# Kernel tuning notes

Measured on AMD Instinct MI355X. Metric: run time of the kernel, lower is better.

Reference implementation:

```python
import jax, jax.numpy as jnp
import numpy as np

NHID, NHEAD, HEAD_DIM, U = 512, 16, 64, 3  # U = unfold_size (hardcoded 3 in original)
B, L = 8, 2048
D = NHEAD * HEAD_DIM  # 1024


def setup_inputs() -> dict:
    key = jax.random.key(0)
    ks = jax.random.split(key, 9)
    s = 0.02
    return {
        "x": jax.random.normal(ks[0], (B, NHID, L, 1), jnp.float32),
        "wq": jax.random.normal(ks[1], (NHID, D), jnp.float32) * s,
        "bq": jnp.zeros((D,), jnp.float32),
        "wk": jax.random.normal(ks[2], (NHID, D), jnp.float32) * s,
        "bk": jnp.zeros((D,), jnp.float32),
        "wv": jax.random.normal(ks[3], (NHID, D), jnp.float32) * s,
        "bv": jnp.zeros((D,), jnp.float32),
        "wo": jax.random.normal(ks[4], (D, NHID), jnp.float32) * s,
        "bo": jnp.zeros((NHID,), jnp.float32),
    }


def _unfold(t):
    # t: (B, D, L). Replicates tf.image.extract_patches (ksize 3, SAME, zero pad)
    # followed by the original's reshape (B,L,1,D,3) -- which reinterprets the
    # window-major flat layout (w*D + c) as (c', w') -- then transpose to
    # (B, D, 3, L) and reshape to (B, nhead, head_dim, 3, L).
    b, d, l = t.shape
    tt = jnp.transpose(t, (0, 2, 1))                  # (B, L, D)
    tp = jnp.pad(tt, ((0, 0), (1, 1), (0, 0)))        # SAME zero padding along L
    p = jnp.stack([tp[:, w:w + l, :] for w in range(U)], axis=2)  # (B, L, 3, D), flat idx = w*D + c
    p = p.reshape(b, l, d, U)                         # faithful reinterpreting reshape
    p = jnp.transpose(p, (0, 2, 3, 1))                # (B, D, 3, L)
    return p.reshape(b, NHEAD, HEAD_DIM, U, l)


def reference(x, wq, bq, wk, bk, wv, bv, wo, bo):
    b, c, l, _ = x.shape
    xs = x[..., 0]                                    # (B, C, L)
    # 1x1 convs (channels_first) == channel matmuls
    q = jnp.einsum('bcl,cd->bdl', xs, wq) + bq[None, :, None]
    k = jnp.einsum('bcl,cd->bdl', xs, wk) + bk[None, :, None]
    v = jnp.einsum('bcl,cd->bdl', xs, wv) + bv[None, :, None]
    q = q.reshape(b, NHEAD, HEAD_DIM, 1, l)           # (B, nh, hd, 1, L)
    k = _unfold(k)                                    # (B, nh, hd, 3, L)
    v = _unfold(v)
    scale = jnp.sqrt(jnp.asarray(HEAD_DIM, x.dtype))
    alphas = jnp.sum(q * k, axis=2, keepdims=True) / scale  # (B, nh, 1, 3, L)
    alphas = jax.nn.softmax(alphas, axis=3)
    att = jnp.sum(alphas * v, axis=3)                 # (B, nh, hd, L)
    # faithful to original: transpose then reinterpreting reshape to (B, D, L)
    att = jnp.transpose(att, (0, 1, 3, 2)).reshape(b, D, l)
    ret = jnp.einsum('bdl,dc->bcl', att, wo) + bo[None, :, None]
    return ret[..., None]                             # (B, nhid, L, 1)
```

## Files before the change

kernel.cpp:

```cpp
#include <hip/hip_runtime.h>

typedef _Float16 f16_t;
typedef _Float16 f16x2 __attribute__((ext_vector_type(2)));
typedef _Float16 f16x8 __attribute__((ext_vector_type(8)));
typedef float floatx4 __attribute__((ext_vector_type(4)));
typedef unsigned int u32;
typedef const __attribute__((address_space(1))) unsigned int* gptr_as1;
typedef __attribute__((address_space(3))) unsigned int* lptr_as3;

#define B_ 8
#define C_ 512
#define L_ 2048
#define D_ 1024
#define H_ 16

static __device__ __forceinline__ f16x2 bc2(u32 v) { return __builtin_bit_cast(f16x2, v); }
static __device__ __forceinline__ u32 cb2(f16x2 v) { return __builtin_bit_cast(u32, v); }

#define SCHEDB() __builtin_amdgcn_sched_barrier(0)

__global__ __launch_bounds__(256) void _MSA1_ktransf2h(const float* __restrict__ in,
                                                       f16_t* __restrict__ out,
                                                       int R, int C) {
  size_t zoff = (size_t)blockIdx.z * R * C;
  in += zoff; out += zoff;
  __shared__ f16_t tile[64][65];
  int r0 = blockIdx.y * 64, c0 = blockIdx.x * 64;
  int t = threadIdx.x;
  #pragma unroll
  for (int i = 0; i < 16; ++i) {
    int idx = t + i * 256;
    int r = idx >> 6, c = idx & 63;
    tile[c][r] = (f16_t)in[(size_t)(r0 + r) * C + (c0 + c)];
  }
  __syncthreads();
  #pragma unroll
  for (int i = 0; i < 16; ++i) {
    int idx = t + i * 256;
    int r = idx >> 6, c = idx & 63;
    out[(size_t)(c0 + r) * R + (r0 + c)] = tile[r][c];
  }
}

__global__ __launch_bounds__(256) void _MSA1_kprep(
    const float* __restrict__ wq, const float* __restrict__ wk,
    const float* __restrict__ wv, const float* __restrict__ wo,
    const float* __restrict__ bq, const float* __restrict__ bk,
    const float* __restrict__ bv,
    f16_t* __restrict__ wT3, f16_t* __restrict__ woT, float* __restrict__ bias3) {
  const int x = blockIdx.x, y = blockIdx.y;
  const int t = threadIdx.x;
  if (x == 128) {
    if (y == 0) {
      for (int i = t; i < 1024; i += 256) {
        bias3[i] = bq[i];
        bias3[1024 + i] = bk[i];
        bias3[2048 + i] = bv[i];
      }
    }
    return;
  }
  __shared__ f16_t tile[64][65];
  const float* in; f16_t* out; int R, C, r0, c0;
  if (y < 3) {
    R = 512; C = 1024;
    in = (y == 0) ? wq : (y == 1) ? wk : wv;
    out = wT3 + (size_t)y * 524288;
    r0 = (x >> 4) * 64; c0 = (x & 15) * 64;
  } else {
    R = 1024; C = 512;
    in = wo; out = woT;
    r0 = (x >> 3) * 64; c0 = (x & 7) * 64;
  }
  #pragma unroll
  for (int i = 0; i < 16; ++i) {
    int idx = t + i * 256;
    int r = idx >> 6, c = idx & 63;
    tile[c][r] = (f16_t)in[(size_t)(r0 + r) * C + (c0 + c)];
  }
  __syncthreads();
  #pragma unroll
  for (int i = 0; i < 16; ++i) {
    int idx = t + i * 256;
    int r = idx >> 6, c = idx & 63;
    out[(size_t)(c0 + r) * R + (r0 + c)] = tile[r][c];
  }
}

template <int K>
__global__ __launch_bounds__(512, 2) void _MSA1_kgemm8(
    const f16_t* __restrict__ A, const f16_t* __restrict__ Bt,
    const float* __restrict__ bias, f16_t* __restrict__ Cd0,
    int M, int N, long sB, long sC) {
  constexpr int KT = K / 64;
  const f16_t* Bz = Bt + (size_t)blockIdx.z * sB;
  const int m0 = blockIdx.y * 256, n0 = blockIdx.x * 256;

  union __align__(16) ShU {
    f16_t AB[8][8192];
    f16_t Ep[64][264];
  };
  __shared__ ShU sh;

  const int t = threadIdx.x;
  const int lane = t & 63;
  const int wid = t >> 6;
  const int wm = wid & 1, wn = wid >> 1;
  const int mh = wm * 128, nh = wn * 64;
  const int fm = lane & 15, fq = lane >> 4;
  const int srcswz = ((t & 3) ^ ((t >> 2) & 3) ^ ((t >> 4) & 3)) * 8;
  const int colf = ((fq ^ (fm & 3) ^ ((fm >> 2) & 3)) * 8);

  floatx4 acc[8][4];
  #pragma unroll
  for (int i = 0; i < 8; ++i)
    #pragma unroll
    for (int j = 0; j < 4; ++j) {
      floatx4 z4 = {0.f, 0.f, 0.f, 0.f};
      acc[i][j] = z4;
    }

  auto SG = [&](int T, int ab, int kk) {
    const int d = T & 1;
    const f16_t* src = ab ? Bz : A;
    const int base0 = ab ? n0 : m0;
    char* ldsb = (char*)&sh.AB[(d * 2 + ab) * 2 + kk][0];
    #pragma unroll
    for (int j = 0; j < 2; ++j) {
      int idx = j * 512 + t;
      int r = idx >> 2;
      const f16_t* g = src + (size_t)(base0 + r) * K + T * 64 + kk * 32 + srcswz;
      __builtin_amdgcn_global_load_lds((gptr_as1)(const void*)g,
          (lptr_as3)(void*)(ldsb + idx * 16), 16, 0, 0);
    }
  };
  auto LDA4 = [&](f16x8* af, int d, int kk, int mhalf) {
    #pragma unroll
    for (int m2 = 0; m2 < 4; ++m2)
      af[m2] = *(const f16x8*)&sh.AB[(d * 2 + 0) * 2 + kk]
                  [(mh + mhalf * 64 + m2 * 16 + fm) * 32 + colf];
  };
  auto LDB4 = [&](f16x8* bf, int d, int kk) {
    #pragma unroll
    for (int nt = 0; nt < 4; ++nt)
      bf[nt] = *(const f16x8*)&sh.AB[(d * 2 + 1) * 2 + kk]
                  [(nh + nt * 16 + fm) * 32 + colf];
  };
  auto MM = [&](const f16x8* af, const f16x8* bf, int mhalf) {
    __builtin_amdgcn_s_setprio(1);
    #pragma unroll
    for (int m2 = 0; m2 < 4; ++m2)
      #pragma unroll
      for (int nt = 0; nt < 4; ++nt)
        acc[mhalf * 4 + m2][nt] = __builtin_amdgcn_mfma_f32_16x16x32_f16(
            af[m2], bf[nt], acc[mhalf * 4 + m2][nt], 0, 0, 0);
    __builtin_amdgcn_s_setprio(0);
  };

  SG(0, 1, 0); SG(0, 0, 0); SG(0, 1, 1); SG(0, 0, 1);
  SG(1, 1, 0); SG(1, 0, 0); SG(1, 1, 1);
  SCHEDB();
  asm volatile("s_waitcnt vmcnt(10)" ::: "memory");
  __builtin_amdgcn_s_barrier();
  SCHEDB();

  f16x8 af[4], bfr[4];
  #pragma unroll
  for (int i = 0; i < KT; ++i) {
    const int d = i & 1;
    LDB4(bfr, d, 0);
    LDA4(af, d, 0, 0);
    SCHEDB();
    __builtin_amdgcn_s_barrier();
    asm volatile("s_waitcnt lgkmcnt(0)" ::: "memory");
    SCHEDB();
    if (i + 1 < KT) SG(i + 1, 0, 1);
    MM(af, bfr, 0);
    LDA4(af, d, 0, 1);
    SCHEDB();
    if (i == KT - 1) {
      asm volatile("s_waitcnt vmcnt(0)" ::: "memory");
    } else {
      asm volatile("s_waitcnt vmcnt(8)" ::: "memory");
    }
    __builtin_amdgcn_s_barrier();
    asm volatile("s_waitcnt lgkmcnt(0)" ::: "memory");
    SCHEDB();
    if (i + 2 < KT) SG(i + 2, 1, 0);
    MM(af, bfr, 1);
    LDB4(bfr, d, 1);
    LDA4(af, d, 1, 0);
    SCHEDB();
    __builtin_amdgcn_s_barrier();
    asm volatile("s_waitcnt lgkmcnt(0)" ::: "memory");
    SCHEDB();
    if (i + 2 < KT) SG(i + 2, 0, 0);
    MM(af, bfr, 0);
    LDA4(af, d, 1, 1);
    SCHEDB();
    if (i + 1 < KT) {
      asm volatile("s_waitcnt vmcnt(8)" ::: "memory");
    }
    __builtin_amdgcn_s_barrier();
    asm volatile("s_waitcnt lgkmcnt(0)" ::: "memory");
    SCHEDB();
    if (i + 2 < KT) SG(i + 2, 1, 1);
    MM(af, bfr, 1);
  }
  __syncthreads();

  f16_t* Cd = Cd0 + (size_t)blockIdx.z * sC;
  #pragma unroll
  for (int p = 0; p < 4; ++p) {
    if (p) __syncthreads();
    if (wm == (p >> 1)) {
      #pragma unroll
      for (int m2 = 0; m2 < 4; ++m2) {
        int mt = (p & 1) * 4 + m2;
        float bv4[4];
        #pragma unroll
        for (int r = 0; r < 4; ++r)
          bv4[r] = bias[m0 + p * 64 + m2 * 16 + fq * 4 + r];
        #pragma unroll
        for (int nt = 0; nt < 4; ++nt) {
          int col = nh + nt * 16 + fm;
          #pragma unroll
          for (int r = 0; r < 4; ++r) {
            int row = m2 * 16 + fq * 4 + r;
            sh.Ep[row][col] = (f16_t)(acc[mt][nt][r] + bv4[r]);
          }
        }
      }
    }
    __syncthreads();
    #pragma unroll
    for (int ii = 0; ii < 8; ++ii) {
      int chunk = ii * 512 + t;
      int row = chunk >> 6, c8 = chunk & 63;
      uint2 val = *(const uint2*)&sh.Ep[row][c8 * 4];
      *(uint2*)&Cd[(size_t)(m0 + p * 64 + row) * N + n0 + c8 * 4] = val;
    }
  }
}

template <bool F32OUT, int K>
__global__ __launch_bounds__(256, 2) void _MSA1_kgemm(
    const f16_t* __restrict__ A, const f16_t* __restrict__ Bt,
    const float* __restrict__ bias, void* __restrict__ Cdv,
    int M, int N, long sA, long sB, long sC) {
  A  += (size_t)blockIdx.z * sA;
  Bt += (size_t)blockIdx.z * sB;
  const int m0 = blockIdx.y * 256, n0 = blockIdx.x * 128;

  union __align__(16) ShU {
    struct { f16_t As[3][256][32]; f16_t Bs[3][128][32]; } ab;
    f16_t Ep[F32OUT ? 1 : 64][132];
  };
  __shared__ ShU sh;

  const int t = threadIdx.x;
  const int lane = t & 63, w = t >> 6;
  const int mh = (w & 1) * 128, nh = (w >> 1) * 64;
  const int fm = lane & 15, fq = lane >> 4;
  const int srcswz = ((t & 3) ^ ((t >> 2) & 3) ^ ((t >> 4) & 3)) * 8;
  const int colf = ((fq ^ (fm & 3) ^ ((fm >> 2) & 3)) * 8);

  floatx4 acc[8][4];
  #pragma unroll
  for (int i = 0; i < 8; ++i)
    #pragma unroll
    for (int j = 0; j < 4; ++j) {
      floatx4 z4 = {0.f, 0.f, 0.f, 0.f};
      acc[i][j] = z4;
    }

  auto STAGE = [&](int kt, int bi) {
    #pragma unroll
    for (int j = 0; j < 4; ++j) {
      int r = (j * 256 + t) >> 2;
      const f16_t* ga = A + (size_t)(m0 + r) * K + kt + srcswz;
      __builtin_amdgcn_global_load_lds((gptr_as1)(const void*)ga,
          (lptr_as3)(void*)((char*)&sh.ab.As[bi][0][0] + j * 4096 + w * 1024), 16, 0, 0);
    }
    #pragma unroll
    for (int j = 0; j < 2; ++j) {
      int r = (j * 256 + t) >> 2;
      const f16_t* gb = Bt + (size_t)(n0 + r) * K + kt + srcswz;
      __builtin_amdgcn_global_load_lds((gptr_as1)(const void*)gb,
          (lptr_as3)(void*)((char*)&sh.ab.Bs[bi][0][0] + j * 4096 + w * 1024), 16, 0, 0);
    }
  };

  STAGE(0, 0);
  STAGE(32, 1);
  SCHEDB();
  asm volatile("s_waitcnt vmcnt(6)" ::: "memory");
  __builtin_amdgcn_s_barrier();
  SCHEDB();

  int bcur = 0;
  for (int kt = 0; kt < K; kt += 32) {
    if (kt + 64 < K) {
      int bi = bcur + 2; if (bi >= 3) bi -= 3;
      STAGE(kt + 64, bi);
    }
    f16x8 af[8], bfr[4];
    #pragma unroll
    for (int mt = 0; mt < 8; ++mt)
      af[mt] = *(const f16x8*)&sh.ab.As[bcur][mh + mt * 16 + fm][colf];
    #pragma unroll
    for (int nt = 0; nt < 4; ++nt)
      bfr[nt] = *(const f16x8*)&sh.ab.Bs[bcur][nh + nt * 16 + fm][colf];
    __builtin_amdgcn_s_setprio(1);
    #pragma unroll
    for (int mt = 0; mt < 8; ++mt)
      #pragma unroll
      for (int nt = 0; nt < 4; ++nt)
        acc[mt][nt] = __builtin_amdgcn_mfma_f32_16x16x32_f16(
            af[mt], bfr[nt], acc[mt][nt], 0, 0, 0);
    __builtin_amdgcn_s_setprio(0);
    if (kt + 32 < K) {
      SCHEDB();
      if (kt + 64 < K)
        asm volatile("s_waitcnt vmcnt(6) lgkmcnt(0)" ::: "memory");
      else
        asm volatile("s_waitcnt vmcnt(0) lgkmcnt(0)" ::: "memory");
      __builtin_amdgcn_s_barrier();
      SCHEDB();
    }
    bcur = (bcur == 2) ? 0 : bcur + 1;
  }
  __syncthreads();

  if (F32OUT) {
    float* Cd = (float*)Cdv + (size_t)blockIdx.z * sC;
    #pragma unroll
    for (int mt = 0; mt < 8; ++mt) {
      float bv4[4];
      #pragma unroll
      for (int r = 0; r < 4; ++r)
        bv4[r] = bias[m0 + mh + mt * 16 + fq * 4 + r];
      #pragma unroll
      for (int nt = 0; nt < 4; ++nt) {
        int col = n0 + nh + nt * 16 + fm;
        #pragma unroll
        for (int r = 0; r < 4; ++r) {
          int row = m0 + mh + mt * 16 + fq * 4 + r;
          Cd[(size_t)row * N + col] = acc[mt][nt][r] + bv4[r];
        }
      }
    }
  } else {
    f16_t* Cd = (f16_t*)Cdv + (size_t)blockIdx.z * sC;
    #pragma unroll
    for (int p = 0; p < 4; ++p) {
      if (p) __syncthreads();
      if ((w & 1) == (p >> 1)) {
        #pragma unroll
        for (int mt2 = 0; mt2 < 4; ++mt2) {
          int mt = (p & 1) * 4 + mt2;
          float bv4[4];
          #pragma unroll
          for (int r = 0; r < 4; ++r)
            bv4[r] = bias[m0 + p * 64 + mt2 * 16 + fq * 4 + r];
          #pragma unroll
          for (int nt = 0; nt < 4; ++nt) {
            int col = nh + nt * 16 + fm;
            #pragma unroll
            for (int r = 0; r < 4; ++r) {
              int row = mt2 * 16 + fq * 4 + r;
              sh.Ep[row][col] = (f16_t)(acc[mt][nt][r] + bv4[r]);
            }
          }
        }
      }
      __syncthreads();
      #pragma unroll
      for (int i = 0; i < 8; ++i) {
        int chunk = i * 256 + t;
        int row = chunk >> 5, c8 = chunk & 31;
        uint2 val = *(const uint2*)&sh.Ep[row][c8 * 4];
        *(uint2*)&Cd[(size_t)(m0 + p * 64 + row) * N + n0 + c8 * 4] = val;
      }
    }
  }
}

__global__ __launch_bounds__(256) void _MSA1_kattn6(const f16_t* __restrict__ qkv,
                                                    f16_t* __restrict__ attT) {
  const int t = threadIdx.x;
  const int lane = t & 63;
  const int wid = __builtin_amdgcn_readfirstlane(t >> 6);
  const int hb = blockIdx.x;
  const int h = hb & 15, b = hb >> 4;
  const int chi = blockIdx.y;
  const int lbase = chi * 256;
  const int l0 = lbase + lane * 4;
  const size_t plane = (size_t)D_ * L_;
  const f16_t* base = qkv + (size_t)b * 3 * plane;

  __shared__ uint2 sred[4][3][64];
  __shared__ __align__(16) f16_t tile2[2048][8];

  const f16_t* qp = base + (size_t)(h * 64 + wid * 16) * L_ + l0;
  const f16_t* kpl = base + plane;
  const f16_t* vpl = base + 2 * plane;
  const int g0 = h * 192 + wid * 48;

  f16x2 sLo[3], sHi[3];
  #pragma unroll
  for (int w = 0; w < 3; ++w) { f16x2 z = {(f16_t)0, (f16_t)0}; sLo[w] = z; sHi[w] = z; }

  #pragma unroll
  for (int dd = 0; dd < 16; ++dd) {
    uint2 qw = *(const uint2*)(qp + (size_t)dd * L_);
    f16x2 qlo = bc2(qw.x), qhi = bc2(qw.y);
    #pragma unroll
    for (int w = 0; w < 3; ++w) {
      int g = g0 + 3 * dd + w;
      int c = g & 1023;
      int o = (g >> 10) - 1;
      uint2 kw = *(const uint2*)(kpl + (size_t)c * L_ + (l0 + o));
      if (o < 0 && l0 == 0) kw.x &= 0xFFFF0000u;
      if (o > 0 && l0 == 2044) kw.y &= 0x0000FFFFu;
      sLo[w] = bc2(kw.x) * qlo + sLo[w];
      sHi[w] = bc2(kw.y) * qhi + sHi[w];
    }
  }
  #pragma unroll
  for (int w = 0; w < 3; ++w) {
    uint2 v; v.x = cb2(sLo[w]); v.y = cb2(sHi[w]);
    sred[wid][w][lane] = v;
  }
  __syncthreads();

  float sc[4][3];
  #pragma unroll
  for (int j = 0; j < 3; ++j) {
    uint2 r0 = sred[0][j][lane], r1 = sred[1][j][lane];
    uint2 r2 = sred[2][j][lane], r3 = sred[3][j][lane];
    f16x2 lo = (bc2(r0.x) + bc2(r1.x)) + (bc2(r2.x) + bc2(r3.x));
    f16x2 hi = (bc2(r0.y) + bc2(r1.y)) + (bc2(r2.y) + bc2(r3.y));
    sc[0][j] = (float)lo.x * 0.125f;
    sc[1][j] = (float)lo.y * 0.125f;
    sc[2][j] = (float)hi.x * 0.125f;
    sc[3][j] = (float)hi.y * 0.125f;
  }
  f16_t ef[4][3];
  #pragma unroll
  for (int li = 0; li < 4; ++li) {
    float mx = fmaxf(sc[li][0], fmaxf(sc[li][1], sc[li][2]));
    float e0 = __expf(sc[li][0] - mx), e1 = __expf(sc[li][1] - mx), e2 = __expf(sc[li][2] - mx);
    float inv = 1.f / (e0 + e1 + e2);
    ef[li][0] = (f16_t)(e0 * inv); ef[li][1] = (f16_t)(e1 * inv); ef[li][2] = (f16_t)(e2 * inv);
  }
  f16x2 eLo[3], eHi[3];
  #pragma unroll
  for (int w = 0; w < 3; ++w) {
    f16x2 a = {ef[0][w], ef[1][w]}; eLo[w] = a;
    f16x2 b2 = {ef[2][w], ef[3][w]}; eHi[w] = b2;
  }

  const int llb = (lane & 7) * 256 + wid * 16;
  const int jcol = lane >> 3;
  #pragma unroll
  for (int dd = 0; dd < 16; ++dd) {
    f16x2 aLo = {(f16_t)0, (f16_t)0}, aHi = {(f16_t)0, (f16_t)0};
    #pragma unroll
    for (int w = 0; w < 3; ++w) {
      int g = g0 + 3 * dd + w;
      int c = g & 1023;
      int o = (g >> 10) - 1;
      uint2 vw = *(const uint2*)(vpl + (size_t)c * L_ + (l0 + o));
      if (o < 0 && l0 == 0) vw.x &= 0xFFFF0000u;
      if (o > 0 && l0 == 2044) vw.y &= 0x0000FFFFu;
      aLo = bc2(vw.x) * eLo[w] + aLo;
      aHi = bc2(vw.y) * eHi[w] + aHi;
    }
    const int llq = llb + dd;
    tile2[llq +   0][jcol] = aLo.x;
    tile2[llq +  64][jcol] = aLo.y;
    tile2[llq + 128][jcol] = aHi.x;
    tile2[llq + 192][jcol] = aHi.y;
  }
  __syncthreads();

  f16_t* ob = attT + (size_t)b * L_ * D_ + h * 64 + chi * 8;
  #pragma unroll
  for (int i = 0; i < 8; ++i) {
    int ll = i * 256 + t;
    uint4 val = *(const uint4*)&tile2[ll][0];
    *(uint4*)(ob + (size_t)ll * D_) = val;
  }
}

extern "C" void kernel_launch(void* const* d_in, const int* in_sizes, int n_in,
                              void* d_out, int out_size, void* d_ws, size_t ws_size,
                              hipStream_t stream) {
  (void)in_sizes; (void)n_in; (void)out_size;
  const float* x  = (const float*)d_in[0];
  const float* wq = (const float*)d_in[1];
  const float* bq = (const float*)d_in[2];
  const float* wk = (const float*)d_in[3];
  const float* bk = (const float*)d_in[4];
  const float* wv = (const float*)d_in[5];
  const float* bv = (const float*)d_in[6];
  const float* wo = (const float*)d_in[7];
  const float* bo = (const float*)d_in[8];
  float* out = (float*)d_out;
  char* ws = (char*)d_ws;

  f16_t* wT3   = (f16_t*)(ws);
  f16_t* woT   = (f16_t*)(ws + 3145728);
  float* bias3 = (float*) (ws + 4194304);
  const size_t SHARED_END = 4210688;

  _MSA1_kprep<<<dim3(129, 4), dim3(256), 0, stream>>>(
      wq, wk, wv, wo, bq, bk, bv, wT3, woT, bias3);

  if (ws_size >= 155205632ull) {
    f16_t* xT    = (f16_t*)(ws + SHARED_END);
    f16_t* qkv   = xT + 8388608ull;
    f16_t* att2T = qkv + 50331648ull;

    _MSA1_ktransf2h<<<dim3(32, 8, B_), dim3(256), 0, stream>>>(x, xT, 512, 2048);
    _MSA1_kgemm8<512><<<dim3(8, 12, B_), dim3(512), 0, stream>>>(
        wT3, xT, bias3, qkv, 3072, 2048,
        (long)(2048 * 512), (long)(3072 * 2048));
    _MSA1_kattn6<<<dim3(128, 8), dim3(256), 0, stream>>>(qkv, att2T);
    _MSA1_kgemm<true, 1024><<<dim3(16, 2, B_), dim3(256), 0, stream>>>(
        woT, att2T, bo, out, 512, 2048,
        0L, (long)(2048 * 1024), (long)(512 * 2048));
  } else {
    f16_t* xTb    = (f16_t*)(ws + SHARED_END);
    f16_t* qkvb   = xTb + 1048576ull;
    f16_t* att2Tb = qkvb + 6291456ull;
    for (int b = 0; b < B_; ++b) {
      const float* xb = x + (size_t)b * C_ * L_;
      _MSA1_ktransf2h<<<dim3(32, 8, 1), dim3(256), 0, stream>>>(xb, xTb, 512, 2048);
      _MSA1_kgemm8<512><<<dim3(8, 12, 1), dim3(512), 0, stream>>>(
          wT3, xTb, bias3, qkvb, 3072, 2048, 0L, 0L);
      _MSA1_kattn6<<<dim3(16, 8), dim3(256), 0, stream>>>(qkvb, att2Tb);
      _MSA1_kgemm<true, 1024><<<dim3(16, 2, 1), dim3(256), 0, stream>>>(
          woT, att2Tb, bo, out + (size_t)b * C_ * L_, 512, 2048, 0L, 0L, 0L);
    }
  }
}
```

Measured before the change: 264.9 us.

## Remap GEMM block order across batches and widen output GEMM to 8 waves

```diff
diff --git a/kernel.cpp b/kernel.cpp
--- a/kernel.cpp
+++ b/kernel.cpp
@@ -93,8 +93,15 @@
     const float* __restrict__ bias, f16_t* __restrict__ Cd0,
     int M, int N, long sB, long sC) {
   constexpr int KT = K / 64;
-  const f16_t* Bz = Bt + (size_t)blockIdx.z * sB;
-  const int m0 = blockIdx.y * 256, n0 = blockIdx.x * 256;
+  int nx, my, zz;
+  if (gridDim.z == 8) {
+    const int o = blockIdx.x + 8 * (blockIdx.y + 12 * blockIdx.z);
+    zz = o & 7; const int r = o >> 3; nx = r & 7; my = r >> 3;
+  } else {
+    nx = blockIdx.x; my = blockIdx.y; zz = blockIdx.z;
+  }
+  const f16_t* Bz = Bt + (size_t)zz * sB;
+  const int m0 = my * 256, n0 = nx * 256;
 
   union __align__(16) ShU {
     f16_t AB[8][8192];
@@ -209,7 +216,7 @@
   }
   __syncthreads();
 
-  f16_t* Cd = Cd0 + (size_t)blockIdx.z * sC;
+  f16_t* Cd = Cd0 + (size_t)zz * sC;
   #pragma unroll
   for (int p = 0; p < 4; ++p) {
     if (p) __syncthreads();
@@ -244,13 +251,20 @@
 }
 
 template <bool F32OUT, int K>
-__global__ __launch_bounds__(256, 2) void _MSA1_kgemm(
+__global__ __launch_bounds__(512, 2) void _MSA1_kgemm(
     const f16_t* __restrict__ A, const f16_t* __restrict__ Bt,
     const float* __restrict__ bias, void* __restrict__ Cdv,
     int M, int N, long sA, long sB, long sC) {
-  A  += (size_t)blockIdx.z * sA;
-  Bt += (size_t)blockIdx.z * sB;
-  const int m0 = blockIdx.y * 256, n0 = blockIdx.x * 128;
+  int nx, my, zz;
+  if (gridDim.z == 8) {
+    const int o = blockIdx.x + 16 * (blockIdx.y + 2 * blockIdx.z);
+    zz = o & 7; const int r = o >> 3; nx = r & 15; my = r >> 4;
+  } else {
+    nx = blockIdx.x; my = blockIdx.y; zz = blockIdx.z;
+  }
+  A  += (size_t)zz * sA;
+  Bt += (size_t)zz * sB;
+  const int m0 = my * 256, n0 = nx * 128;
 
   union __align__(16) ShU {
     struct { f16_t As[3][256][32]; f16_t Bs[3][128][32]; } ab;
@@ -260,14 +274,14 @@
 
   const int t = threadIdx.x;
   const int lane = t & 63, w = t >> 6;
-  const int mh = (w & 1) * 128, nh = (w >> 1) * 64;
+  const int mh = (w & 3) * 64, nh = (w >> 2) * 64;
   const int fm = lane & 15, fq = lane >> 4;
   const int srcswz = ((t & 3) ^ ((t >> 2) & 3) ^ ((t >> 4) & 3)) * 8;
   const int colf = ((fq ^ (fm & 3) ^ ((fm >> 2) & 3)) * 8);
 
-  floatx4 acc[8][4];
-  #pragma unroll
-  for (int i = 0; i < 8; ++i)
+  floatx4 acc[4][4];
+  #pragma unroll
+  for (int i = 0; i < 4; ++i)
     #pragma unroll
     for (int j = 0; j < 4; ++j) {
       floatx4 z4 = {0.f, 0.f, 0.f, 0.f};
@@ -276,25 +290,25 @@
 
   auto STAGE = [&](int kt, int bi) {
     #pragma unroll
-    for (int j = 0; j < 4; ++j) {
-      int r = (j * 256 + t) >> 2;
+    for (int j = 0; j < 2; ++j) {
+      int idx = j * 512 + t;
+      int r = idx >> 2;
       const f16_t* ga = A + (size_t)(m0 + r) * K + kt + srcswz;
       __builtin_amdgcn_global_load_lds((gptr_as1)(const void*)ga,
-          (lptr_as3)(void*)((char*)&sh.ab.As[bi][0][0] + j * 4096 + w * 1024), 16, 0, 0);
-    }
-    #pragma unroll
-    for (int j = 0; j < 2; ++j) {
-      int r = (j * 256 + t) >> 2;
+          (lptr_as3)(void*)((char*)&sh.ab.As[bi][0][0] + j * 8192 + w * 1024), 16, 0, 0);
+    }
+    {
+      int r = t >> 2;
       const f16_t* gb = Bt + (size_t)(n0 + r) * K + kt + srcswz;
       __builtin_amdgcn_global_load_lds((gptr_as1)(const void*)gb,
-          (lptr_as3)(void*)((char*)&sh.ab.Bs[bi][0][0] + j * 4096 + w * 1024), 16, 0, 0);
+          (lptr_as3)(void*)((char*)&sh.ab.Bs[bi][0][0] + w * 1024), 16, 0, 0);
     }
   };
 
   STAGE(0, 0);
   STAGE(32, 1);
   SCHEDB();
-  asm volatile("s_waitcnt vmcnt(6)" ::: "memory");
+  asm volatile("s_waitcnt vmcnt(3)" ::: "memory");
   __builtin_amdgcn_s_barrier();
   SCHEDB();
 
@@ -304,16 +318,16 @@
       int bi = bcur + 2; if (bi >= 3) bi -= 3;
       STAGE(kt + 64, bi);
     }
-    f16x8 af[8], bfr[4];
-    #pragma unroll
-    for (int mt = 0; mt < 8; ++mt)
+    f16x8 af[4], bfr[4];
+    #pragma unroll
+    for (int mt = 0; mt < 4; ++mt)
       af[mt] = *(const f16x8*)&sh.ab.As[bcur][mh + mt * 16 + fm][colf];
     #pragma unroll
     for (int nt = 0; nt < 4; ++nt)
       bfr[nt] = *(const f16x8*)&sh.ab.Bs[bcur][nh + nt * 16 + fm][colf];
     __builtin_amdgcn_s_setprio(1);
     #pragma unroll
-    for (int mt = 0; mt < 8; ++mt)
+    for (int mt = 0; mt < 4; ++mt)
       #pragma unroll
       for (int nt = 0; nt < 4; ++nt)
         acc[mt][nt] = __builtin_amdgcn_mfma_f32_16x16x32_f16(
@@ -322,7 +336,7 @@
     if (kt + 32 < K) {
       SCHEDB();
       if (kt + 64 < K)
-        asm volatile("s_waitcnt vmcnt(6) lgkmcnt(0)" ::: "memory");
+        asm volatile("s_waitcnt vmcnt(3) lgkmcnt(0)" ::: "memory");
       else
         asm volatile("s_waitcnt vmcnt(0) lgkmcnt(0)" ::: "memory");
       __builtin_amdgcn_s_barrier();
@@ -333,9 +347,9 @@
   __syncthreads();
 
   if (F32OUT) {
-    float* Cd = (float*)Cdv + (size_t)blockIdx.z * sC;
-    #pragma unroll
-    for (int mt = 0; mt < 8; ++mt) {
+    float* Cd = (float*)Cdv + (size_t)zz * sC;
+    #pragma unroll
+    for (int mt = 0; mt < 4; ++mt) {
       float bv4[4];
       #pragma unroll
       for (int r = 0; r < 4; ++r)
@@ -351,14 +365,13 @@
       }
     }
   } else {
-    f16_t* Cd = (f16_t*)Cdv + (size_t)blockIdx.z * sC;
+    f16_t* Cd = (f16_t*)Cdv + (size_t)zz * sC;
     #pragma unroll
     for (int p = 0; p < 4; ++p) {
       if (p) __syncthreads();
       if ((w & 1) == (p >> 1)) {
         #pragma unroll
         for (int mt2 = 0; mt2 < 4; ++mt2) {
-          int mt = (p & 1) * 4 + mt2;
           float bv4[4];
           #pragma unroll
           for (int r = 0; r < 4; ++r)
@@ -369,7 +382,7 @@
             #pragma unroll
             for (int r = 0; r < 4; ++r) {
               int row = mt2 * 16 + fq * 4 + r;
-              sh.Ep[row][col] = (f16_t)(acc[mt][nt][r] + bv4[r]);
+              sh.Ep[row & (F32OUT ? 0 : 63)][col] = (f16_t)(acc[mt2][nt][r] + bv4[r]);
             }
           }
         }
@@ -377,9 +390,9 @@
       __syncthreads();
       #pragma unroll
       for (int i = 0; i < 8; ++i) {
-        int chunk = i * 256 + t;
+        int chunk = i * 256 + (t & 255);
         int row = chunk >> 5, c8 = chunk & 31;
-        uint2 val = *(const uint2*)&sh.Ep[row][c8 * 4];
+        uint2 val = *(const uint2*)&sh.Ep[row & (F32OUT ? 0 : 63)][c8 * 4];
         *(uint2*)&Cd[(size_t)(m0 + p * 64 + row) * N + n0 + c8 * 4] = val;
       }
     }
@@ -528,7 +541,7 @@
         wT3, xT, bias3, qkv, 3072, 2048,
         (long)(2048 * 512), (long)(3072 * 2048));
     _MSA1_kattn6<<<dim3(128, 8), dim3(256), 0, stream>>>(qkv, att2T);
-    _MSA1_kgemm<true, 1024><<<dim3(16, 2, B_), dim3(256), 0, stream>>>(
+    _MSA1_kgemm<true, 1024><<<dim3(16, 2, B_), dim3(512), 0, stream>>>(
         woT, att2T, bo, out, 512, 2048,
         0L, (long)(2048 * 1024), (long)(512 * 2048));
   } else {
@@ -541,7 +554,7 @@
       _MSA1_kgemm8<512><<<dim3(8, 12, 1), dim3(512), 0, stream>>>(
           wT3, xTb, bias3, qkvb, 3072, 2048, 0L, 0L);
       _MSA1_kattn6<<<dim3(16, 8), dim3(256), 0, stream>>>(qkvb, att2Tb);
-      _MSA1_kgemm<true, 1024><<<dim3(16, 2, 1), dim3(256), 0, stream>>>(
+      _MSA1_kgemm<true, 1024><<<dim3(16, 2, 1), dim3(512), 0, stream>>>(
           woT, att2Tb, bo, out + (size_t)b * C_ * L_, 512, 2048, 0L, 0L, 0L);
     }
   }
```

New measurement: 256.6 us. 1.03x faster.
